# Kernel optimization log

Hardware: AMD Instinct MI355X
Metric: run time of the kernel (lower is better)

The kernel has to match this reference:

```python
import functools
import jax, jax.numpy as jnp
import numpy as np

INPUT_DIM = 3
NUM_LEVELS = 8
LEVEL_DIM = 2
PER_LEVEL_SCALE = 2
BASE_RESOLUTION = 16
LOG2_HASHMAP_SIZE = 19
BATCH = 2_097_152

PRIMES = np.array([1, 2654435761, 805459861], dtype=np.uint32)


def _level_offsets():
    max_params = 2 ** LOG2_HASHMAP_SIZE
    offsets, offset = [], 0
    for i in range(NUM_LEVELS):
        res = int(np.ceil(BASE_RESOLUTION * PER_LEVEL_SCALE ** i))
        params = min(max_params, res ** INPUT_DIM)
        params = int(np.ceil(params / 32) * 32)
        offset += params
        offsets.append(offset)
    return offsets  # cumulative, last entry = total table rows


OFFSETS = _level_offsets()
TABLE_ROWS = OFFSETS[-1]  # 2920448


def setup_inputs() -> dict:
    key = jax.random.key(0)
    k1, k2 = jax.random.split(key)
    inputs = jax.random.uniform(k1, (BATCH, INPUT_DIM), dtype=jnp.float32)
    embeddings = jax.random.normal(k2, (TABLE_ROWS, LEVEL_DIM), dtype=jnp.float32) * 0.05
    return {"inputs": inputs, "embeddings": embeddings}


def reference(inputs, embeddings):
    primes = jnp.asarray(PRIMES)  # uint32; multiply wraps mod 2^32, matching `& 0xFFFFFFFF`
    outs = []
    for i in range(NUM_LEVELS):
        res = int(np.ceil(BASE_RESOLUTION * PER_LEVEL_SCALE ** i))
        offset = 0 if i == 0 else OFFSETS[i - 1]
        params_in_level = OFFSETS[i] - offset
        x = inputs * res  # [N, 3], nonnegative
        xi = jnp.floor(x)  # == trunc for x >= 0, matches .long()
        xf = x - jax.lax.stop_gradient(xi)  # fractional part, grad flows only through x
        bin_mask = xf < 0.5  # eval-mode stochastic-corner: pick nearest corner
        xi_u = xi.astype(jnp.uint32)
        neigs = jnp.where(bin_mask, xi_u, xi_u + jnp.uint32(1))  # [N, 3]
        h = neigs * primes  # uint32 wraparound multiply
        hashed = functools.reduce(jnp.bitwise_xor, [h[..., d] for d in range(INPUT_DIM)])
        hash_ids = (hashed % jnp.uint32(params_in_level)).astype(jnp.int32) + offset  # [N]
        feats = embeddings[hash_ids]  # [N, level_dim] irregular gather
        w = jnp.where(bin_mask, xf, 1.0 - xf)  # [N, 3]
        outs.append(jnp.concatenate([feats, w], axis=-1))  # [N, level_dim + 3]
    outs.append(inputs)
    return jnp.concatenate(outs, axis=-1)  # [N, num_levels*(level_dim+3)+3] = [N, 43]
```

## Files before the change

kernel.cpp:

```cpp
#include <hip/hip_runtime.h>

#define NLEV 8
#define COLS 43
#define TPB1 256
#define TPB  64

typedef float v4f __attribute__((ext_vector_type(4)));
typedef float v2f __attribute__((ext_vector_type(2)));

__device__ __constant__ unsigned off_c[NLEV]  = {0u, 4096u, 36864u, 299008u,
                                                 823296u, 1347584u, 1871872u, 2396160u};
__device__ __constant__ unsigned mask_c[NLEV] = {4095u, 32767u, 262143u, 524287u,
                                                 524287u, 524287u, 524287u, 524287u};

__global__ __launch_bounds__(TPB1) void gather_kernel(
    const float* __restrict__ inputs,
    const float2* __restrict__ emb,
    v2f* __restrict__ ws,
    int N)
{
    const int level = blockIdx.x & 7;
    const int i = (blockIdx.x >> 3) * TPB1 + threadIdx.x;
    if (i >= N) return;

    const float x0 = __builtin_nontemporal_load(&inputs[3 * i + 0]);
    const float x1 = __builtin_nontemporal_load(&inputs[3 * i + 1]);
    const float x2 = __builtin_nontemporal_load(&inputs[3 * i + 2]);

    const float res = (float)(16 << level);
    const float a = x0 * res, b = x1 * res, c = x2 * res;
    const float fa = floorf(a), fb = floorf(b), fc = floorf(c);
    const float ga = a - fa, gb = b - fb, gc = c - fc;
    const unsigned na = (unsigned)fa + (ga < 0.5f ? 0u : 1u);
    const unsigned nb = (unsigned)fb + (gb < 0.5f ? 0u : 1u);
    const unsigned nc = (unsigned)fc + (gc < 0.5f ? 0u : 1u);
    const unsigned h = na ^ (nb * 2654435761u) ^ (nc * 805459861u);
    const unsigned id = (h & mask_c[level]) + off_c[level];

    const float2 f = emb[id];
    v2f v; v.x = f.x; v.y = f.y;
    __builtin_nontemporal_store(v, ws + (size_t)level * N + i);
}

__global__ __launch_bounds__(TPB) void assemble_kernel(
    const float* __restrict__ inputs,
    const v2f* __restrict__ ws,
    float* __restrict__ out,
    int N)
{
    __shared__ __align__(16) float lds[TPB * COLS];
    const int tid = threadIdx.x;
    const int i = blockIdx.x * TPB + tid;

    if (i < N) {
        v2f f[NLEV];
        #pragma unroll
        for (int L = 0; L < NLEV; ++L)
            f[L] = __builtin_nontemporal_load(ws + (size_t)L * N + i);

        const float x0 = inputs[3 * i + 0];
        const float x1 = inputs[3 * i + 1];
        const float x2 = inputs[3 * i + 2];
        float* row = &lds[tid * COLS];

        #pragma unroll
        for (int L = 0; L < NLEV; ++L) {
            const float res = (float)(16 << L);
            const float a = x0 * res, b = x1 * res, c = x2 * res;
            const float ga = a - floorf(a), gb = b - floorf(b), gc = c - floorf(c);
            row[5 * L + 2] = ga < 0.5f ? ga : 1.0f - ga;
            row[5 * L + 3] = gb < 0.5f ? gb : 1.0f - gb;
            row[5 * L + 4] = gc < 0.5f ? gc : 1.0f - gc;
        }
        #pragma unroll
        for (int L = 0; L < NLEV; ++L) {
            row[5 * L + 0] = f[L].x;
            row[5 * L + 1] = f[L].y;
        }
        row[40] = x0;
        row[41] = x1;
        row[42] = x2;
    }
    __syncthreads();

    const long long tile_base = (long long)blockIdx.x * (TPB * COLS);
    if ((blockIdx.x + 1) * TPB <= N) {
        v4f* __restrict__ out4 = (v4f*)(out + tile_base);
        const v4f* l4 = (const v4f*)lds;
        const int NV = TPB * COLS / 4;
        #pragma unroll
        for (int j = 0; j < 10; ++j) {
            const int k = tid + j * TPB;
            __builtin_nontemporal_store(l4[k], &out4[k]);
        }
        const int k = tid + 10 * TPB;
        if (k < NV)
            __builtin_nontemporal_store(l4[k], &out4[k]);
    } else {
        const int valid = N - blockIdx.x * TPB;
        const int NT = valid * COLS;
        for (int k = tid; k < NT; k += TPB)
            out[tile_base + k] = lds[k];
    }
}

__global__ __launch_bounds__(TPB) void hashgrid_kernel(
    const float* __restrict__ inputs,
    const float2* __restrict__ emb,
    float* __restrict__ out,
    int N)
{
    __shared__ __align__(16) float lds[TPB * COLS];
    const int tid = threadIdx.x;
    const int i = blockIdx.x * TPB + tid;

    if (i < N) {
        const float x0 = inputs[3 * i + 0];
        const float x1 = inputs[3 * i + 1];
        const float x2 = inputs[3 * i + 2];

        unsigned id[NLEV];
        float ga[NLEV], gb[NLEV], gc[NLEV];
        bool  ma[NLEV], mb[NLEV], mc[NLEV];
        #pragma unroll
        for (int L = 0; L < NLEV; ++L) {
            const float res = (float)(16 << L);
            const float a = x0 * res, b = x1 * res, c = x2 * res;
            const float fa = floorf(a), fb = floorf(b), fc = floorf(c);
            ga[L] = a - fa; gb[L] = b - fb; gc[L] = c - fc;
            ma[L] = ga[L] < 0.5f; mb[L] = gb[L] < 0.5f; mc[L] = gc[L] < 0.5f;
            const unsigned na = (unsigned)fa + (ma[L] ? 0u : 1u);
            const unsigned nb = (unsigned)fb + (mb[L] ? 0u : 1u);
            const unsigned nc = (unsigned)fc + (mc[L] ? 0u : 1u);
            const unsigned h = na ^ (nb * 2654435761u) ^ (nc * 805459861u);
            id[L] = (h & mask_c[L]) + off_c[L];
        }
        float2 f[NLEV];
        #pragma unroll
        for (int L = 0; L < NLEV; ++L) f[L] = emb[id[L]];

        float* row = &lds[tid * COLS];
        #pragma unroll
        for (int L = 0; L < NLEV; ++L) {
            row[5 * L + 2] = ma[L] ? ga[L] : 1.0f - ga[L];
            row[5 * L + 3] = mb[L] ? gb[L] : 1.0f - gb[L];
            row[5 * L + 4] = mc[L] ? gc[L] : 1.0f - gc[L];
        }
        row[40] = x0;
        row[41] = x1;
        row[42] = x2;
        #pragma unroll
        for (int L = 0; L < NLEV; ++L) {
            row[5 * L + 0] = f[L].x;
            row[5 * L + 1] = f[L].y;
        }
    }
    __syncthreads();

    const long long tile_base = (long long)blockIdx.x * (TPB * COLS);
    if ((blockIdx.x + 1) * TPB <= N) {
        v4f* __restrict__ out4 = (v4f*)(out + tile_base);
        const v4f* l4 = (const v4f*)lds;
        const int NV = TPB * COLS / 4;
        #pragma unroll
        for (int j = 0; j < 10; ++j) {
            const int k = tid + j * TPB;
            __builtin_nontemporal_store(l4[k], &out4[k]);
        }
        const int k = tid + 10 * TPB;
        if (k < NV)
            __builtin_nontemporal_store(l4[k], &out4[k]);
    } else {
        const int valid = N - blockIdx.x * TPB;
        const int NT = valid * COLS;
        for (int k = tid; k < NT; k += TPB)
            out[tile_base + k] = lds[k];
    }
}

extern "C" void kernel_launch(void* const* d_in, const int* in_sizes, int n_in,
                              void* d_out, int out_size, void* d_ws, size_t ws_size,
                              hipStream_t stream) {
    const float*  inputs = (const float*)d_in[0];
    const float2* emb    = (const float2*)d_in[1];
    float* out = (float*)d_out;
    const int N = in_sizes[0] / 3;

    const size_t ws_need = (size_t)NLEV * N * sizeof(float2);
    if (d_ws != nullptr && ws_size >= ws_need) {
        const int chunks = (N + TPB1 - 1) / TPB1;
        gather_kernel<<<chunks * NLEV, TPB1, 0, stream>>>(inputs, emb, (v2f*)d_ws, N);
        const int grid2 = (N + TPB - 1) / TPB;
        assemble_kernel<<<grid2, TPB, 0, stream>>>(inputs, (const v2f*)d_ws, out, N);
    } else {
        const int grid = (N + TPB - 1) / TPB;
        hashgrid_kernel<<<grid, TPB, 0, stream>>>(inputs, emb, out, N);
    }
}
```

Measured before the change: 554.8 us.

## Partition big-level gathers by table slice and fuse small-level gathers into assemble

The three small levels (tables up to 262K rows) are now gathered directly in the assemble kernel instead of going through the workspace. For the five large levels, each of 8 blocks per chunk handles only the lookups whose hash falls in its own 64K-row slice (hash bits 16-18). This keeps each block's random gathers within a 512KB region for better cache locality. The trade-off is that every gather block recomputes all five hashes and only performs about one-eighth of the loads, which adds ALU work and branch divergence.

```diff
diff --git a/kernel.cpp b/kernel.cpp
--- a/kernel.cpp
+++ b/kernel.cpp
@@ -1,6 +1,7 @@
 #include <hip/hip_runtime.h>
 
 #define NLEV 8
+#define NBIG 5
 #define COLS 43
 #define TPB1 256
 #define TPB  64
@@ -13,37 +14,53 @@
 __device__ __constant__ unsigned mask_c[NLEV] = {4095u, 32767u, 262143u, 524287u,
                                                  524287u, 524287u, 524287u, 524287u};
 
-__global__ __launch_bounds__(TPB1) void gather_kernel(
+__global__ __launch_bounds__(TPB1) void gather_big(
     const float* __restrict__ inputs,
     const float2* __restrict__ emb,
     v2f* __restrict__ ws,
     int N)
 {
-    const int level = blockIdx.x & 7;
-    const int i = (blockIdx.x >> 3) * TPB1 + threadIdx.x;
+    const unsigned p = (unsigned)blockIdx.x & 7u;
+    const int i = (int)((unsigned)blockIdx.x >> 3) * TPB1 + (int)threadIdx.x;
     if (i >= N) return;
 
     const float x0 = __builtin_nontemporal_load(&inputs[3 * i + 0]);
     const float x1 = __builtin_nontemporal_load(&inputs[3 * i + 1]);
     const float x2 = __builtin_nontemporal_load(&inputs[3 * i + 2]);
 
-    const float res = (float)(16 << level);
-    const float a = x0 * res, b = x1 * res, c = x2 * res;
-    const float fa = floorf(a), fb = floorf(b), fc = floorf(c);
-    const float ga = a - fa, gb = b - fb, gc = c - fc;
-    const unsigned na = (unsigned)fa + (ga < 0.5f ? 0u : 1u);
-    const unsigned nb = (unsigned)fb + (gb < 0.5f ? 0u : 1u);
-    const unsigned nc = (unsigned)fc + (gc < 0.5f ? 0u : 1u);
-    const unsigned h = na ^ (nb * 2654435761u) ^ (nc * 805459861u);
-    const unsigned id = (h & mask_c[level]) + off_c[level];
-
-    const float2 f = emb[id];
-    v2f v; v.x = f.x; v.y = f.y;
-    __builtin_nontemporal_store(v, ws + (size_t)level * N + i);
+    unsigned idw[NBIG];
+    bool own[NBIG];
+    #pragma unroll
+    for (int k = 0; k < NBIG; ++k) {
+        const int L = k + 3;
+        const float res = (float)(16 << L);
+        const float a = x0 * res, b = x1 * res, c = x2 * res;
+        const float fa = floorf(a), fb = floorf(b), fc = floorf(c);
+        const float ga = a - fa, gb = b - fb, gc = c - fc;
+        const unsigned na = (unsigned)fa + (ga < 0.5f ? 0u : 1u);
+        const unsigned nb = (unsigned)fb + (gb < 0.5f ? 0u : 1u);
+        const unsigned nc = (unsigned)fc + (gc < 0.5f ? 0u : 1u);
+        const unsigned h = na ^ (nb * 2654435761u) ^ (nc * 805459861u);
+        idw[k] = h & 524287u;
+        own[k] = (idw[k] >> 16) == p;
+    }
+    float2 f[NBIG];
+    #pragma unroll
+    for (int k = 0; k < NBIG; ++k) {
+        if (own[k]) f[k] = emb[idw[k] + off_c[k + 3]];
+    }
+    #pragma unroll
+    for (int k = 0; k < NBIG; ++k) {
+        if (own[k]) {
+            v2f v; v.x = f[k].x; v.y = f[k].y;
+            __builtin_nontemporal_store(v, ws + (size_t)k * N + i);
+        }
+    }
 }
 
 __global__ __launch_bounds__(TPB) void assemble_kernel(
     const float* __restrict__ inputs,
+    const float2* __restrict__ emb,
     const v2f* __restrict__ ws,
     float* __restrict__ out,
     int N)
@@ -53,16 +70,30 @@
     const int i = blockIdx.x * TPB + tid;
 
     if (i < N) {
-        v2f f[NLEV];
-        #pragma unroll
-        for (int L = 0; L < NLEV; ++L)
-            f[L] = __builtin_nontemporal_load(ws + (size_t)L * N + i);
+        v2f fb[NBIG];
+        #pragma unroll
+        for (int k = 0; k < NBIG; ++k)
+            fb[k] = __builtin_nontemporal_load(ws + (size_t)k * N + i);
 
         const float x0 = inputs[3 * i + 0];
         const float x1 = inputs[3 * i + 1];
         const float x2 = inputs[3 * i + 2];
+
+        float2 fs[3];
+        #pragma unroll
+        for (int L = 0; L < 3; ++L) {
+            const float res = (float)(16 << L);
+            const float a = x0 * res, b = x1 * res, c = x2 * res;
+            const float fa = floorf(a), fb2 = floorf(b), fc = floorf(c);
+            const float ga = a - fa, gb = b - fb2, gc = c - fc;
+            const unsigned na = (unsigned)fa + (ga < 0.5f ? 0u : 1u);
+            const unsigned nb = (unsigned)fb2 + (gb < 0.5f ? 0u : 1u);
+            const unsigned nc = (unsigned)fc + (gc < 0.5f ? 0u : 1u);
+            const unsigned h = na ^ (nb * 2654435761u) ^ (nc * 805459861u);
+            fs[L] = emb[(h & mask_c[L]) + off_c[L]];
+        }
+
         float* row = &lds[tid * COLS];
-
         #pragma unroll
         for (int L = 0; L < NLEV; ++L) {
             const float res = (float)(16 << L);
@@ -73,9 +104,14 @@
             row[5 * L + 4] = gc < 0.5f ? gc : 1.0f - gc;
         }
         #pragma unroll
-        for (int L = 0; L < NLEV; ++L) {
-            row[5 * L + 0] = f[L].x;
-            row[5 * L + 1] = f[L].y;
+        for (int L = 0; L < 3; ++L) {
+            row[5 * L + 0] = fs[L].x;
+            row[5 * L + 1] = fs[L].y;
+        }
+        #pragma unroll
+        for (int k = 0; k < NBIG; ++k) {
+            row[5 * (k + 3) + 0] = fb[k].x;
+            row[5 * (k + 3) + 1] = fb[k].y;
         }
         row[40] = x0;
         row[41] = x1;
@@ -186,12 +222,12 @@
     float* out = (float*)d_out;
     const int N = in_sizes[0] / 3;
 
-    const size_t ws_need = (size_t)NLEV * N * sizeof(float2);
+    const size_t ws_need = (size_t)NBIG * N * sizeof(float2);
     if (d_ws != nullptr && ws_size >= ws_need) {
         const int chunks = (N + TPB1 - 1) / TPB1;
-        gather_kernel<<<chunks * NLEV, TPB1, 0, stream>>>(inputs, emb, (v2f*)d_ws, N);
+        gather_big<<<chunks * 8, TPB1, 0, stream>>>(inputs, emb, (v2f*)d_ws, N);
         const int grid2 = (N + TPB - 1) / TPB;
-        assemble_kernel<<<grid2, TPB, 0, stream>>>(inputs, (const v2f*)d_ws, out, N);
+        assemble_kernel<<<grid2, TPB, 0, stream>>>(inputs, emb, (const v2f*)d_ws, out, N);
     } else {
         const int grid = (N + TPB - 1) / TPB;
         hashgrid_kernel<<<grid, TPB, 0, stream>>>(inputs, emb, out, N);
```

New measurement: 668.4 us. 20.5% more time.
